# Kernel optimization log

Hardware: AMD Instinct MI355X
Metric: run time of the kernel (lower is better)

Reference implementation:

```python
import jax, jax.numpy as jnp
import numpy as np

DEPTH = 10
NUM_LEAVES = 2 ** DEPTH  # 1024


def setup_inputs() -> dict:
    key = jax.random.key(0)
    k1, k2, k3, k4 = jax.random.split(key, 4)
    B, C, T = 4096, 512, 4096
    x = jax.random.normal(k1, (B, C), dtype=jnp.float32)
    # thresholds = 6*rand - 3, as in __init__
    thresholds = 6.0 * jax.random.uniform(k2, (T, NUM_LEAVES - 1), dtype=jnp.float32) - 3.0
    ordinals = jax.random.randint(k3, (T, NUM_LEAVES - 1), 0, C, dtype=jnp.int32)
    weights = jax.random.normal(k4, (T, NUM_LEAVES), dtype=jnp.float32)
    return {"x": x, "thresholds": thresholds, "ordinals": ordinals, "weights": weights}


def reference(x, thresholds, ordinals, weights):
    """Random hinge forest forward.

    For each sample b and tree t: traverse the perfect binary tree of depth
    DEPTH.  At node n, margin m = x[b, ordinals[t, n]] - thresholds[t, n];
    go right (child 2n+2) if m > 0 else left (child 2n+1).  Track the signed
    margin of minimum magnitude along the path.  Output is
    |min-margin| * weights[t, leaf].
    """
    B = x.shape[0]
    T = thresholds.shape[0]
    tr = jnp.arange(T)  # [T], broadcasts against [B, T] node indices
    node = jnp.zeros((B, T), dtype=jnp.int32)
    minm = jnp.full((B, T), jnp.inf, dtype=x.dtype)
    for _ in range(DEPTH):
        thr = thresholds[tr, node]                      # [B, T]
        ordv = ordinals[tr, node]                       # [B, T] feature ids
        feat = jnp.take_along_axis(x, ordv, axis=1)     # [B, T]
        m = feat - thr
        minm = jnp.where(jnp.abs(m) < jnp.abs(minm), m, minm)
        node = 2 * node + 1 + (m > 0).astype(jnp.int32)
    leaf = node - (NUM_LEAVES - 1)                      # [B, T] in [0, 2^depth)
    w = weights[tr, leaf]                               # [B, T]
    return jnp.abs(minm) * w
```

## Files before the change

### kernel.cpp

```cpp
#include <hip/hip_runtime.h>
#include <hip/hip_fp16.h>

#define BB 4096
#define CC 512
#define TT 4096
#define NN 1023
#define NL 1024


__device__ __forceinline__ unsigned pack_node(float th, int o) {
    return ((unsigned)o << 23) | (unsigned)__half_as_ushort(__float2half(th));
}

__global__ __launch_bounds__(256)
void pack_trees(const float* __restrict__ thr, const int* __restrict__ ord,
                const float* __restrict__ wts, unsigned* __restrict__ pk_lo,
                uint2* __restrict__ g7, uint2* __restrict__ g8,
                uint4* __restrict__ tails) {
    int t = blockIdx.x, tid = threadIdx.x;
    const float* tr = thr + (size_t)t * NN;
    const int*   oo = ord + (size_t)t * NN;
    if (tid < 128) {
        unsigned* plo = pk_lo + ((size_t)t << 7);
        plo[tid] = (tid == 0) ? 0u : pack_node(tr[tid - 1], oo[tid - 1]);
    }
    if (tid < 64) {
        int j = tid;
        g7[((size_t)t << 6) + j] =
            make_uint2(pack_node(tr[127 + 2 * j], oo[127 + 2 * j]),
                       pack_node(tr[128 + 2 * j], oo[128 + 2 * j]));
    }
    if (tid < 128) {
        int j = tid;
        g8[((size_t)t << 7) + j] =
            make_uint2(pack_node(tr[255 + 2 * j], oo[255 + 2 * j]),
                       pack_node(tr[256 + 2 * j], oo[256 + 2 * j]));
    }
    int i = tid;
    int nL = 511 + 2 * i, nR = 512 + 2 * i;
    unsigned ndL = pack_node(tr[nL], oo[nL]);
    unsigned ndR = pack_node(tr[nR], oo[nR]);
    float4 w4 = *(const float4*)(wts + ((size_t)t << 10) + 4 * i);
    unsigned w01 = (unsigned)__half_as_ushort(__float2half(w4.x)) |
                   ((unsigned)__half_as_ushort(__float2half(w4.y)) << 16);
    unsigned w23 = (unsigned)__half_as_ushort(__float2half(w4.z)) |
                   ((unsigned)__half_as_ushort(__float2half(w4.w)) << 16);
    tails[((size_t)t << 8) + i] = make_uint4(ndL, ndR, w01, w23);
}

__global__ __launch_bounds__(256)
void pack_x16(const float* __restrict__ x, unsigned short* __restrict__ xt16) {
    __shared__ float tile[64][65];
    int tx = threadIdx.x & 63, ty = threadIdx.x >> 6;
    int b0 = blockIdx.x * 64;
    int c0 = blockIdx.y * 64;
    #pragma unroll
    for (int i = 0; i < 16; ++i) {
        int rr = i * 4 + ty;
        tile[rr][tx] = x[(size_t)(b0 + rr) * CC + c0 + tx];
    }
    __syncthreads();
    #pragma unroll
    for (int i = 0; i < 16; ++i) {
        int cr = i * 4 + ty;
        xt16[(size_t)(c0 + cr) * BB + b0 + tx] =
            __half_as_ushort(__float2half(tile[tx][cr]));
    }
}

typedef unsigned short u16x2 __attribute__((ext_vector_type(2)));

static __device__ __forceinline__ unsigned psub_f16x2(unsigned a, unsigned b) {
    __half2 ah, bh;
    __builtin_memcpy(&ah, &a, 4);
    __builtin_memcpy(&bh, &b, 4);
    __half2 r = ah - bh;
    unsigned u; __builtin_memcpy(&u, &r, 4); return u;
}
static __device__ __forceinline__ unsigned pmin_u16x2(unsigned a, unsigned b) {
    u16x2 av, bv;
    __builtin_memcpy(&av, &a, 4);
    __builtin_memcpy(&bv, &b, 4);
    u16x2 m = __builtin_elementwise_min(av, bv);
    unsigned u; __builtin_memcpy(&u, &m, 4); return u;
}
static __device__ __forceinline__ float f16lo(unsigned u) {
    return __half2float(__ushort_as_half((unsigned short)(u & 0xffffu)));
}
static __device__ __forceinline__ float f16hi(unsigned u) {
    return __half2float(__ushort_as_half((unsigned short)(u >> 16)));
}

#define LDS_BYTES 163840

typedef __attribute__((address_space(1))) const void gv_t;
typedef __attribute__((address_space(3))) void lv_t;

__global__ __launch_bounds__(1024, 1)
void rhf_main(const unsigned* __restrict__ pk_lo, const uint2* __restrict__ g7g,
              const uint2* __restrict__ g8g, const uint4* __restrict__ tails,
              const unsigned short* __restrict__ xt16, float* __restrict__ out) {
    extern __shared__ char smem[];
    const char*     xsb = (const char*)smem;
    unsigned*       trl = (unsigned*)(smem + 65536);
    float*          res = (float*)(smem + 131072);

    const int tid  = threadIdx.x;
    const int lane = tid & 63;
    const int wv   = tid >> 6;
    const int bi   = blockIdx.x;
    const int tb    = ((bi & 7) << 2) + ((bi >> 3) >> 6);
    const int panel = (bi >> 3) & 63;
    const int lane2 = lane << 1;

    {
        const char* s = (const char*)pk_lo + ((size_t)(tb * 128 + wv * 8) << 9) + lane * 16;
        char* d = (char*)trl + wv * 4096 + lane * 16;
        #pragma unroll
        for (int q = 0; q < 4; ++q)
            __builtin_amdgcn_global_load_lds((gv_t*)(s + q * 1024),
                                             (lv_t*)(d + q * 1024), 16, 0, 0);
    }

    {
        const unsigned short* src = xt16 + (size_t)panel * 64;
        #pragma unroll
        for (int k = 0; k < 4; ++k) {
            int i4 = k * 1024 + tid;
            int c  = i4 >> 3;
            int o8 = (i4 & 7) << 3;
            uint4 v = *(const uint4*)(src + (size_t)c * BB + o8);
            *(uint4*)((char*)smem + ((size_t)i4 << 4)) = v;
        }
    }
    __syncthreads();

    const int t0 = tb * 128 + wv * 8;
    const unsigned* pkw = trl + wv * 1024;

    auto evalpair = [&](unsigned nd_a, unsigned nd_b, unsigned& amin,
                        unsigned& r_a, unsigned& r_b) {
        unsigned thv2 = (nd_a & 0xffffu) | (nd_b << 16);
        unsigned short fa = *(const unsigned short*)(xsb + (nd_a >> 16) + lane2);
        unsigned short fb = *(const unsigned short*)(xsb + (nd_b >> 16) + lane2);
        unsigned feat2 = (unsigned)fa | ((unsigned)fb << 16);
        unsigned mb = psub_f16x2(feat2, thv2);
        amin = pmin_u16x2(amin, mb & 0x7fff7fffu);
        r_a = ((mb >> 15) & 1u) ^ 1u;
        r_b = (mb >> 31) ^ 1u;
    };

    unsigned amin[4];
    int      sl[8];
    unsigned nd[8];
    unsigned r[8];
    #pragma unroll
    for (int p = 0; p < 4; ++p) amin[p] = 0x7c007c00u;
    #pragma unroll
    for (int c = 0; c < 8; ++c) { sl[c] = 1; nd[c] = pkw[c * 128 + 1]; }

    #pragma unroll
    for (int d = 0; d < 6; ++d) {
        uint2 ch[8];
        #pragma unroll
        for (int c = 0; c < 8; ++c)
            ch[c] = *(const uint2*)(pkw + c * 128 + 2 * sl[c]);
        #pragma unroll
        for (int p = 0; p < 4; ++p)
            evalpair(nd[2 * p], nd[2 * p + 1], amin[p], r[2 * p], r[2 * p + 1]);
        #pragma unroll
        for (int c = 0; c < 8; ++c) {
            sl[c] = 2 * sl[c] + (int)r[c];
            nd[c] = r[c] ? ch[c].y : ch[c].x;
        }
    }

    {
        uint2 q[8];
        #pragma unroll
        for (int c = 0; c < 8; ++c)
            q[c] = g7g[((size_t)(t0 + c) << 6) + (sl[c] - 64)];
        #pragma unroll
        for (int p = 0; p < 4; ++p)
            evalpair(nd[2 * p], nd[2 * p + 1], amin[p], r[2 * p], r[2 * p + 1]);
        #pragma unroll
        for (int c = 0; c < 8; ++c) {
            sl[c] = 2 * sl[c] + (int)r[c];
            nd[c] = r[c] ? q[c].y : q[c].x;
        }
    }

    {
        uint2 q[8];
        #pragma unroll
        for (int c = 0; c < 8; ++c)
            q[c] = g8g[((size_t)(t0 + c) << 7) + (sl[c] - 128)];
        #pragma unroll
        for (int p = 0; p < 4; ++p)
            evalpair(nd[2 * p], nd[2 * p + 1], amin[p], r[2 * p], r[2 * p + 1]);
        #pragma unroll
        for (int c = 0; c < 8; ++c) {
            sl[c] = 2 * sl[c] + (int)r[c];
            nd[c] = r[c] ? q[c].y : q[c].x;
        }
    }

    unsigned wsel[8];
    {
        uint4 e[8];
        #pragma unroll
        for (int c = 0; c < 8; ++c)
            e[c] = tails[((size_t)(t0 + c) << 8) + (sl[c] - 256)];
        #pragma unroll
        for (int p = 0; p < 4; ++p)
            evalpair(nd[2 * p], nd[2 * p + 1], amin[p], r[2 * p], r[2 * p + 1]);
        #pragma unroll
        for (int c = 0; c < 8; ++c) {
            nd[c]   = r[c] ? e[c].y : e[c].x;
            wsel[c] = r[c] ? e[c].w : e[c].z;
        }
    }

    {
        #pragma unroll
        for (int p = 0; p < 4; ++p)
            evalpair(nd[2 * p], nd[2 * p + 1], amin[p], r[2 * p], r[2 * p + 1]);
        #pragma unroll
        for (int c = 0; c < 8; ++c) {
            unsigned short wb = (unsigned short)(r[c] ? (wsel[c] >> 16) : (wsel[c] & 0xffffu));
            float am = (c & 1) ? f16hi(amin[c >> 1]) : f16lo(amin[c >> 1]);
            float o  = am * __half2float(__ushort_as_half(wb));
            int col = wv * 8 + c;
            res[(lane << 7) + ((col + lane) & 127)] = o;
        }
    }
    __syncthreads();

    float* obase = out + (size_t)(tb * 128);
    #pragma unroll
    for (int k = 0; k < 8; ++k) {
        int idx = k * 1024 + tid;
        int rr = idx >> 7, cc = idx & 127;
        float v = res[(rr << 7) + ((cc + rr) & 127)];
        obase[((size_t)panel * 64 + rr) * TT + cc] = v;
    }
}

#define F_SP 32
#define F_TG 16
#define F_GROUPS 8
#define F_TPB (F_TG * F_GROUPS)
#define F_NPANELS (BB / F_SP)
#define F_LDS 147456

__global__ __launch_bounds__(512, 1)
void rhf_fallback(const float* __restrict__ x, const float* __restrict__ thr_g,
                  const int* __restrict__ ord_g, const float* __restrict__ wts,
                  float* __restrict__ out) {
    extern __shared__ char smem[];
    float*        xs  = (float*)(smem);
    unsigned int* pk  = (unsigned int*)(smem + 65536);
    float*        res = (float*)(smem + 131072);
    const int tid = threadIdx.x, s = tid & 31, slot = tid >> 5;
    const int panel = blockIdx.x & (F_NPANELS - 1), tb = blockIdx.x >> 7;
    const float* xbase = x + (size_t)panel * F_SP * CC;
    #pragma unroll
    for (int k = 0; k < (F_SP * CC) / 512; ++k) {
        int idx = k * 512 + tid, r = idx >> 9, c = idx & 511;
        xs[(c << 5) + r] = xbase[r * CC + c];
    }
    float4 pthr[8]; int4 pord[8]; float tthr[3]; int tord[3];
    auto prefetch = [&](int g) {
        const size_t base = (size_t)(tb * F_TPB + g * F_TG + slot) * NN;
        #pragma unroll
        for (int k = 0; k < 8; ++k) {
            int j = k * 128 + 4 * s;
            if (j < 1020) { pthr[k] = *(const float4*)(thr_g + base + j);
                            pord[k] = *(const int4*)(ord_g + base + j); }
            else { tthr[0]=thr_g[base+1020]; tord[0]=ord_g[base+1020];
                   tthr[1]=thr_g[base+1021]; tord[1]=ord_g[base+1021];
                   tthr[2]=thr_g[base+1022]; tord[2]=ord_g[base+1022]; }
        }
    };
    auto pack1 = [](float f, int o) -> unsigned int {
        return ((unsigned int)o << 16) | (unsigned int)__half_as_ushort(__float2half(f));
    };
    auto commit = [&]() {
        unsigned int* pt = pk + (slot << 10);
        #pragma unroll
        for (int k = 0; k < 8; ++k) {
            int j = k * 128 + 4 * s;
            if (j < 1020) {
                pt[1+j+0]=pack1(pthr[k].x,pord[k].x); pt[1+j+1]=pack1(pthr[k].y,pord[k].y);
                pt[1+j+2]=pack1(pthr[k].z,pord[k].z); pt[1+j+3]=pack1(pthr[k].w,pord[k].w);
            } else { pt[1+1020]=pack1(tthr[0],tord[0]); pt[1+1021]=pack1(tthr[1],tord[1]);
                     pt[1+1022]=pack1(tthr[2],tord[2]); }
        }
    };
    prefetch(0);
    __builtin_amdgcn_sched_barrier(0);
    for (int g = 0; g < F_GROUPS; ++g) {
        __syncthreads();
        commit();
        __syncthreads();
        if (g + 1 < F_GROUPS) prefetch(g + 1);
        __builtin_amdgcn_sched_barrier(0);
        const int t = tb * F_TPB + g * F_TG + slot;
        const unsigned int* pkt = pk + (slot << 10);
        float minm = __builtin_inff();
        int sl = 1;
        unsigned int cur = pkt[1];
        #pragma unroll
        for (int d = 0; d < 10; ++d) {
            uint2 ch;
            if (d < 9) ch = *(const uint2*)(pkt + 2 * sl);
            float thv = __half2float(__ushort_as_half((unsigned short)(cur & 0xffffu)));
            int orv = (int)(cur >> 16);
            float feat = xs[(orv << 5) + s];
            float m = feat - thv;
            bool take = fabsf(m) < fabsf(minm);
            minm = take ? m : minm;
            int right = (m > 0.0f) ? 1 : 0;
            sl = 2 * sl + right;
            if (d < 9) cur = right ? ch.y : ch.x;
        }
        int leaf = sl - NL;
        float w = wts[(size_t)t * NL + leaf];
        int col = g * F_TG + slot;
        res[(s << 7) + ((col + s) & 127)] = fabsf(minm) * w;
    }
    __syncthreads();
    float* obase = out + (size_t)panel * F_SP * TT + (size_t)tb * F_TPB;
    #pragma unroll
    for (int k = 0; k < (F_SP * F_TPB) / 512; ++k) {
        int idx = k * 512 + tid, rr = idx >> 7, c = idx & 127;
        obase[(size_t)rr * TT + c] = res[(rr << 7) + ((c + rr) & 127)];
    }
}

extern "C" void kernel_launch(void* const* d_in, const int* in_sizes, int n_in,
                              void* d_out, int out_size, void* d_ws, size_t ws_size,
                              hipStream_t stream) {
    const float* x    = (const float*)d_in[0];
    const float* thr  = (const float*)d_in[1];
    const int*   ordv = (const int*)d_in[2];
    const float* wts  = (const float*)d_in[3];
    float*       out  = (float*)d_out;

    const size_t pk_bytes   = (size_t)TT * 128 * 4;
    const size_t g7_bytes   = (size_t)TT * 64 * 8;
    const size_t g8_bytes   = (size_t)TT * 128 * 8;
    const size_t tail_bytes = (size_t)TT * 256 * 16;
    const size_t xt_bytes   = (size_t)CC * BB * 2;

    if (d_ws && ws_size >= pk_bytes + g7_bytes + g8_bytes + tail_bytes + xt_bytes) {
        char* p = (char*)d_ws;
        unsigned*       pk_lo = (unsigned*)p;            p += pk_bytes;
        uint2*          g7    = (uint2*)p;               p += g7_bytes;
        uint2*          g8    = (uint2*)p;               p += g8_bytes;
        uint4*          tails = (uint4*)p;               p += tail_bytes;
        unsigned short* xt16  = (unsigned short*)p;
        pack_trees<<<TT, 256, 0, stream>>>(thr, ordv, wts, pk_lo, g7, g8, tails);
        dim3 gx(BB / 64, CC / 64);
        pack_x16<<<gx, 256, 0, stream>>>(x, xt16);
        (void)hipFuncSetAttribute((const void*)rhf_main,
                            hipFuncAttributeMaxDynamicSharedMemorySize, LDS_BYTES);
        rhf_main<<<2048, 1024, LDS_BYTES, stream>>>(pk_lo, g7, g8, tails, xt16, out);
    } else {
        (void)hipFuncSetAttribute((const void*)rhf_fallback,
                            hipFuncAttributeMaxDynamicSharedMemorySize, F_LDS);
        rhf_fallback<<<F_NPANELS * (TT / F_TPB), 512, F_LDS, stream>>>(x, thr, ordv, wts, out);
    }
}
```

Before: 111.6 us.

## Mirror packed tree layout, store outputs directly, and async-load x into LDS

```diff
diff --git a/kernel.cpp b/kernel.cpp
--- a/kernel.cpp
+++ b/kernel.cpp
@@ -22,30 +22,36 @@
     const int*   oo = ord + (size_t)t * NN;
     if (tid < 128) {
         unsigned* plo = pk_lo + ((size_t)t << 7);
-        plo[tid] = (tid == 0) ? 0u : pack_node(tr[tid - 1], oo[tid - 1]);
+        if (tid == 0) plo[0] = 0u;
+        else {
+            int d = 31 - __clz(tid);
+            int n = 3 * (1 << d) - 2 - tid;
+            plo[tid] = pack_node(tr[n], oo[n]);
+        }
     }
     if (tid < 64) {
-        int j = tid;
-        g7[((size_t)t << 6) + j] =
-            make_uint2(pack_node(tr[127 + 2 * j], oo[127 + 2 * j]),
-                       pack_node(tr[128 + 2 * j], oo[128 + 2 * j]));
+        int k = tid;
+        g7[((size_t)t << 6) + k] =
+            make_uint2(pack_node(tr[254 - 2 * k], oo[254 - 2 * k]),
+                       pack_node(tr[253 - 2 * k], oo[253 - 2 * k]));
     }
     if (tid < 128) {
-        int j = tid;
-        g8[((size_t)t << 7) + j] =
-            make_uint2(pack_node(tr[255 + 2 * j], oo[255 + 2 * j]),
-                       pack_node(tr[256 + 2 * j], oo[256 + 2 * j]));
-    }
-    int i = tid;
-    int nL = 511 + 2 * i, nR = 512 + 2 * i;
-    unsigned ndL = pack_node(tr[nL], oo[nL]);
-    unsigned ndR = pack_node(tr[nR], oo[nR]);
-    float4 w4 = *(const float4*)(wts + ((size_t)t << 10) + 4 * i);
-    unsigned w01 = (unsigned)__half_as_ushort(__float2half(w4.x)) |
-                   ((unsigned)__half_as_ushort(__float2half(w4.y)) << 16);
-    unsigned w23 = (unsigned)__half_as_ushort(__float2half(w4.z)) |
-                   ((unsigned)__half_as_ushort(__float2half(w4.w)) << 16);
-    tails[((size_t)t << 8) + i] = make_uint4(ndL, ndR, w01, w23);
+        int k = tid;
+        g8[((size_t)t << 7) + k] =
+            make_uint2(pack_node(tr[510 - 2 * k], oo[510 - 2 * k]),
+                       pack_node(tr[509 - 2 * k], oo[509 - 2 * k]));
+    }
+    {
+        int i = tid;
+        unsigned A = pack_node(tr[1022 - 2 * i], oo[1022 - 2 * i]);
+        unsigned B = pack_node(tr[1021 - 2 * i], oo[1021 - 2 * i]);
+        float4 w4 = *(const float4*)(wts + ((size_t)t << 10) + (1020 - 4 * i));
+        unsigned w01 = (unsigned)__half_as_ushort(__float2half(w4.w)) |
+                       ((unsigned)__half_as_ushort(__float2half(w4.z)) << 16);
+        unsigned w23 = (unsigned)__half_as_ushort(__float2half(w4.y)) |
+                       ((unsigned)__half_as_ushort(__float2half(w4.x)) << 16);
+        tails[((size_t)t << 8) + i] = make_uint4(A, B, w01, w23);
+    }
 }
 
 __global__ __launch_bounds__(256)
@@ -91,7 +97,7 @@
     return __half2float(__ushort_as_half((unsigned short)(u >> 16)));
 }
 
-#define LDS_BYTES 163840
+#define LDS_BYTES 131072
 
 typedef __attribute__((address_space(1))) const void gv_t;
 typedef __attribute__((address_space(3))) void lv_t;
@@ -101,9 +107,8 @@
               const uint2* __restrict__ g8g, const uint4* __restrict__ tails,
               const unsigned short* __restrict__ xt16, float* __restrict__ out) {
     extern __shared__ char smem[];
-    const char*     xsb = (const char*)smem;
-    unsigned*       trl = (unsigned*)(smem + 65536);
-    float*          res = (float*)(smem + 131072);
+    const char* xsb = (const char*)smem;
+    unsigned*   trl = (unsigned*)(smem + 65536);
 
     const int tid  = threadIdx.x;
     const int lane = tid & 63;
@@ -129,8 +134,9 @@
             int i4 = k * 1024 + tid;
             int c  = i4 >> 3;
             int o8 = (i4 & 7) << 3;
-            uint4 v = *(const uint4*)(src + (size_t)c * BB + o8);
-            *(uint4*)((char*)smem + ((size_t)i4 << 4)) = v;
+            __builtin_amdgcn_global_load_lds((gv_t*)(src + (size_t)c * BB + o8),
+                                             (lv_t*)((char*)smem + ((size_t)i4 << 4)),
+                                             16, 0, 0);
         }
     }
     __syncthreads();
@@ -139,21 +145,21 @@
     const unsigned* pkw = trl + wv * 1024;
 
     auto evalpair = [&](unsigned nd_a, unsigned nd_b, unsigned& amin,
-                        unsigned& r_a, unsigned& r_b) {
-        unsigned thv2 = (nd_a & 0xffffu) | (nd_b << 16);
-        unsigned short fa = *(const unsigned short*)(xsb + (nd_a >> 16) + lane2);
-        unsigned short fb = *(const unsigned short*)(xsb + (nd_b >> 16) + lane2);
-        unsigned feat2 = (unsigned)fa | ((unsigned)fb << 16);
+                        bool& s_a, bool& s_b) {
+        unsigned thv2 = __builtin_amdgcn_perm(nd_b, nd_a, 0x05040100u);
+        unsigned fa = *(const unsigned short*)(xsb + (nd_a >> 16) + lane2);
+        unsigned fb = *(const unsigned short*)(xsb + (nd_b >> 16) + lane2);
+        unsigned feat2 = fa | (fb << 16);
         unsigned mb = psub_f16x2(feat2, thv2);
         amin = pmin_u16x2(amin, mb & 0x7fff7fffu);
-        r_a = ((mb >> 15) & 1u) ^ 1u;
-        r_b = (mb >> 31) ^ 1u;
+        s_a = (short)(mb & 0xffffu) < 0;
+        s_b = (int)mb < 0;
     };
 
     unsigned amin[4];
-    int      sl[8];
+    unsigned sl[8];
     unsigned nd[8];
-    unsigned r[8];
+    bool     s[8];
     #pragma unroll
     for (int p = 0; p < 4; ++p) amin[p] = 0x7c007c00u;
     #pragma unroll
@@ -167,11 +173,11 @@
             ch[c] = *(const uint2*)(pkw + c * 128 + 2 * sl[c]);
         #pragma unroll
         for (int p = 0; p < 4; ++p)
-            evalpair(nd[2 * p], nd[2 * p + 1], amin[p], r[2 * p], r[2 * p + 1]);
-        #pragma unroll
-        for (int c = 0; c < 8; ++c) {
-            sl[c] = 2 * sl[c] + (int)r[c];
-            nd[c] = r[c] ? ch[c].y : ch[c].x;
+            evalpair(nd[2 * p], nd[2 * p + 1], amin[p], s[2 * p], s[2 * p + 1]);
+        #pragma unroll
+        for (int c = 0; c < 8; ++c) {
+            sl[c] = 2 * sl[c] + (s[c] ? 1u : 0u);
+            nd[c] = s[c] ? ch[c].y : ch[c].x;
         }
     }
 
@@ -182,11 +188,11 @@
             q[c] = g7g[((size_t)(t0 + c) << 6) + (sl[c] - 64)];
         #pragma unroll
         for (int p = 0; p < 4; ++p)
-            evalpair(nd[2 * p], nd[2 * p + 1], amin[p], r[2 * p], r[2 * p + 1]);
-        #pragma unroll
-        for (int c = 0; c < 8; ++c) {
-            sl[c] = 2 * sl[c] + (int)r[c];
-            nd[c] = r[c] ? q[c].y : q[c].x;
+            evalpair(nd[2 * p], nd[2 * p + 1], amin[p], s[2 * p], s[2 * p + 1]);
+        #pragma unroll
+        for (int c = 0; c < 8; ++c) {
+            sl[c] = 2 * sl[c] + (s[c] ? 1u : 0u);
+            nd[c] = s[c] ? q[c].y : q[c].x;
         }
     }
 
@@ -197,11 +203,11 @@
             q[c] = g8g[((size_t)(t0 + c) << 7) + (sl[c] - 128)];
         #pragma unroll
         for (int p = 0; p < 4; ++p)
-            evalpair(nd[2 * p], nd[2 * p + 1], amin[p], r[2 * p], r[2 * p + 1]);
-        #pragma unroll
-        for (int c = 0; c < 8; ++c) {
-            sl[c] = 2 * sl[c] + (int)r[c];
-            nd[c] = r[c] ? q[c].y : q[c].x;
+            evalpair(nd[2 * p], nd[2 * p + 1], amin[p], s[2 * p], s[2 * p + 1]);
+        #pragma unroll
+        for (int c = 0; c < 8; ++c) {
+            sl[c] = 2 * sl[c] + (s[c] ? 1u : 0u);
+            nd[c] = s[c] ? q[c].y : q[c].x;
         }
     }
 
@@ -213,36 +219,28 @@
             e[c] = tails[((size_t)(t0 + c) << 8) + (sl[c] - 256)];
         #pragma unroll
         for (int p = 0; p < 4; ++p)
-            evalpair(nd[2 * p], nd[2 * p + 1], amin[p], r[2 * p], r[2 * p + 1]);
-        #pragma unroll
-        for (int c = 0; c < 8; ++c) {
-            nd[c]   = r[c] ? e[c].y : e[c].x;
-            wsel[c] = r[c] ? e[c].w : e[c].z;
-        }
-    }
-
-    {
-        #pragma unroll
-        for (int p = 0; p < 4; ++p)
-            evalpair(nd[2 * p], nd[2 * p + 1], amin[p], r[2 * p], r[2 * p + 1]);
-        #pragma unroll
-        for (int c = 0; c < 8; ++c) {
-            unsigned short wb = (unsigned short)(r[c] ? (wsel[c] >> 16) : (wsel[c] & 0xffffu));
+            evalpair(nd[2 * p], nd[2 * p + 1], amin[p], s[2 * p], s[2 * p + 1]);
+        #pragma unroll
+        for (int c = 0; c < 8; ++c) {
+            nd[c]   = s[c] ? e[c].y : e[c].x;
+            wsel[c] = s[c] ? e[c].w : e[c].z;
+        }
+    }
+
+    {
+        #pragma unroll
+        for (int p = 0; p < 4; ++p)
+            evalpair(nd[2 * p], nd[2 * p + 1], amin[p], s[2 * p], s[2 * p + 1]);
+        float o[8];
+        #pragma unroll
+        for (int c = 0; c < 8; ++c) {
+            unsigned short wb = (unsigned short)(s[c] ? (wsel[c] >> 16) : (wsel[c] & 0xffffu));
             float am = (c & 1) ? f16hi(amin[c >> 1]) : f16lo(amin[c >> 1]);
-            float o  = am * __half2float(__ushort_as_half(wb));
-            int col = wv * 8 + c;
-            res[(lane << 7) + ((col + lane) & 127)] = o;
-        }
-    }
-    __syncthreads();
-
-    float* obase = out + (size_t)(tb * 128);
-    #pragma unroll
-    for (int k = 0; k < 8; ++k) {
-        int idx = k * 1024 + tid;
-        int rr = idx >> 7, cc = idx & 127;
-        float v = res[(rr << 7) + ((cc + rr) & 127)];
-        obase[((size_t)panel * 64 + rr) * TT + cc] = v;
+            o[c] = am * __half2float(__ushort_as_half(wb));
+        }
+        float* orow = out + ((size_t)panel * 64 + lane) * TT + t0;
+        *(float4*)(orow)     = make_float4(o[0], o[1], o[2], o[3]);
+        *(float4*)(orow + 4) = make_float4(o[4], o[5], o[6], o[7]);
     }
 }
 
```

Result: slower. 259.8 us (+132.9%).
